# Performance work log

Measured on AMD Instinct MI355X. Metric: run time of the kernel, lower is better.

Reference implementation:

```python
import jax, jax.numpy as jnp
import numpy as np

LN_EPS = 1e-5

def _layernorm(x, gamma, beta):
    mu = jnp.mean(x, axis=-1, keepdims=True)
    var = jnp.var(x, axis=-1, keepdims=True)
    return (x - mu) * jax.lax.rsqrt(var + LN_EPS) * gamma + beta

def setup_inputs() -> dict:
    key = jax.random.key(0)
    ks = jax.random.split(key, 4)
    B, s, d, L = 8, 192, 512, 8
    h = 2048  # embed_dim * 2
    return {
        "lags": jax.random.normal(ks[0], (B, s, d, L), dtype=jnp.float32),
        "gamma1": jnp.ones((d,), jnp.float32),
        "beta1": jnp.zeros((d,), jnp.float32),
        "W1": jax.random.normal(ks[1], (d, h), jnp.float32) * (1.0 / np.sqrt(d)),
        "b1": jnp.zeros((h,), jnp.float32),
        "W2": jax.random.normal(ks[2], (h, d), jnp.float32) * (1.0 / np.sqrt(h)),
        "b2": jnp.zeros((d,), jnp.float32),
        "gamma3": jnp.ones((d,), jnp.float32),
        "beta3": jnp.zeros((d,), jnp.float32),
    }

def reference(lags, gamma1, beta1, W1, b1, W2, b2, gamma3, beta3):
    B, s, d, L = lags.shape
    # (B, s, d, L) -> (B, s, L, d) -> (B, S=s*L, d)
    x = jnp.transpose(lags, (0, 1, 3, 2)).reshape(B, s * L, d)
    scale = 1.0 / jnp.sqrt(jnp.asarray(d, x.dtype))
    # single-head, unprojected attention: scores = X X^T / sqrt(d)
    scores = jnp.einsum('bqd,bkd->bqk', x, x) * scale  # [B, S, S]
    attn = jax.nn.softmax(scores, axis=-1)
    attn_out = jnp.einsum('bqk,bkd->bqd', attn, x)
    q = _layernorm(x + attn_out, gamma1, beta1)
    ff = jnp.dot(jax.nn.gelu(jnp.dot(q, W1) + b1, approximate=False), W2) + b2
    out = _layernorm(q + ff, gamma3, beta3)
    # (B, S, d) -> (B, s, L, d) -> (B, s, d, L)
    return jnp.transpose(out.reshape(B, s, L, d), (0, 1, 3, 2))
```

## Files before the change

### kernel.cpp

```cpp
#include <hip/hip_runtime.h>
#include <hip/hip_bf16.h>
#include <math.h>

#define B_ 8
#define S_ 192
#define D_ 512
#define L_ 8
#define SQ 1536
#define H_ 2048
#define NROW (B_*SQ)
#define SCALE_QK 0.04419417382415922f

typedef unsigned short ushort_t;
typedef unsigned int uint_t;
typedef __attribute__((ext_vector_type(8))) short bf16x8;
typedef __attribute__((ext_vector_type(4))) float f32x4;

__device__ __forceinline__ float bfu2f(ushort_t u) { return __uint_as_float((unsigned)u << 16); }
__device__ __forceinline__ ushort_t f2bfu(float f) {
  __hip_bfloat16 h = __float2bfloat16(f);
  return *reinterpret_cast<ushort_t*>(&h);
}

__device__ __forceinline__ float gelu_fast(float x) {
  float z = fabsf(x) * 0.70710678118654752f;
  float t = __builtin_amdgcn_rcpf(fmaf(0.3275911f, z, 1.0f));
  float p = fmaf(1.061405429f, t, -1.453152027f);
  p = fmaf(p, t, 1.421413741f);
  p = fmaf(p, t, -0.284496736f);
  p = fmaf(p, t, 0.254829592f);
  p = p * t;
  float e = __expf(-z * z);
  float erfz = fmaf(-p, e, 1.0f);
  float s = (x >= 0.0f) ? erfz : -erfz;
  return 0.5f * x * (1.0f + s);
}

__device__ __forceinline__ void gl_lds16(const ushort_t* g, ushort_t* l) {
  __builtin_amdgcn_global_load_lds(
      (const __attribute__((address_space(1))) unsigned int*)g,
      (__attribute__((address_space(3))) unsigned int*)l, 16, 0, 0);
}

#define VMWAIT(N) asm volatile("s_waitcnt vmcnt(" #N ")" ::: "memory")

__global__ __launch_bounds__(256) void k_build_x_f(const float* __restrict__ lags,
                                                   float* __restrict__ x,
                                                   ushort_t* __restrict__ x_bf) {
  __shared__ float tile[512][9];
  const int tid = threadIdx.x;
  const float* in = lags + (size_t)blockIdx.x * 4096;
  #pragma unroll
  for (int it = 0; it < 4; ++it) {
    int f = (tid + it * 256) * 4;
    float4 v = *reinterpret_cast<const float4*>(in + f);
    int k = f >> 3, l0 = f & 7;
    tile[k][l0] = v.x; tile[k][l0 + 1] = v.y; tile[k][l0 + 2] = v.z; tile[k][l0 + 3] = v.w;
  }
  __syncthreads();
  const int l = tid >> 5, kbase = tid & 31;
  const size_t r = (size_t)blockIdx.x * 8 + l;
  #pragma unroll
  for (int j = 0; j < 16; ++j) {
    int k = kbase + 32 * j;
    float v = tile[k][l];
    x[r * D_ + k] = v;
    x_bf[r * D_ + k] = f2bfu(v);
  }
}

__global__ __launch_bounds__(256) void k_xt(const ushort_t* __restrict__ x_bf,
                                            ushort_t* __restrict__ xT) {
  __shared__ ushort_t tile[64][65];
  int t0 = blockIdx.x * 64, d0 = blockIdx.y * 64;
  const ushort_t* X = x_bf + (size_t)blockIdx.z * SQ * D_;
  ushort_t* XT = xT + (size_t)blockIdx.z * SQ * D_;
  for (int i = threadIdx.x; i < 4096; i += 256) {
    int tt = i >> 6, dd = i & 63;
    tile[dd][tt] = X[(size_t)(t0 + tt) * D_ + d0 + dd];
  }
  __syncthreads();
  for (int i = threadIdx.x; i < 4096; i += 256) {
    int dd = i >> 6, tt = i & 63;
    XT[(size_t)(d0 + dd) * SQ + t0 + tt] = tile[dd][tt];
  }
}

__global__ __launch_bounds__(256) void k_wt(const float* __restrict__ W,
                                            ushort_t* __restrict__ Wt,
                                            int K, int N) {
  __shared__ ushort_t tile[64][65];
  int n0 = blockIdx.x * 64, k0 = blockIdx.y * 64;
  for (int i = threadIdx.x; i < 4096; i += 256) {
    int kk = i >> 6, nn = i & 63;
    tile[nn][kk] = f2bfu(W[(size_t)(k0 + kk) * N + n0 + nn]);
  }
  __syncthreads();
  for (int i = threadIdx.x; i < 4096; i += 256) {
    int nn = i >> 6, kk = i & 63;
    Wt[(size_t)(n0 + nn) * K + k0 + kk] = tile[nn][kk];
  }
}

template<int MODE>
__global__ __launch_bounds__(256) void k_gemm(const ushort_t* __restrict__ A,
                                              const ushort_t* __restrict__ Bt,
                                              const float* __restrict__ bias,
                                              void* __restrict__ Cout,
                                              int M, int K, int N,
                                              size_t sAz, size_t sBz, size_t sCz,
                                              float scale) {
  A  += (size_t)blockIdx.z * sAz;
  Bt += (size_t)blockIdx.z * sBz;
  __shared__ ushort_t As0[128 * 64];
  __shared__ ushort_t As1[128 * 64];
  __shared__ ushort_t Bs0[128 * 64];
  __shared__ ushort_t Bs1[128 * 64];
  const int tid = threadIdx.x;
  const int m0 = blockIdx.y * 128, n0 = blockIdx.x * 128;
  const int w = tid >> 6, lane = tid & 63;
  const int wr = w >> 1, wc = w & 1;
  const int l15 = lane & 15, quad = lane >> 4;
  const int lrow8 = lane >> 3;
  const int cg = ((lane & 7) ^ lrow8) * 8;
  const int xsw = l15 & 7;
  const int lbase = (w * 32) * 64;
  const size_t sK8 = (size_t)8 * K;

  f32x4 acc[4][4];
  if (MODE <= 1) {
    #pragma unroll
    for (int nj = 0; nj < 4; ++nj) {
      float bv = bias[n0 + wc * 64 + nj * 16 + l15];
      #pragma unroll
      for (int mi = 0; mi < 4; ++mi) acc[mi][nj] = (f32x4){bv, bv, bv, bv};
    }
  } else {
    #pragma unroll
    for (int nj = 0; nj < 4; ++nj)
      #pragma unroll
      for (int mi = 0; mi < 4; ++mi) acc[mi][nj] = (f32x4){0.f, 0.f, 0.f, 0.f};
  }

  const ushort_t* gA = A  + (size_t)(m0 + w * 32 + lrow8) * K + cg;
  const ushort_t* gB = Bt + (size_t)(n0 + w * 32 + lrow8) * K + cg;

#define STAGE(AS, BS) do {                                                  \
    ushort_t* la_ = &AS[lbase]; ushort_t* lb_ = &BS[lbase];                 \
    _Pragma("unroll")                                                       \
    for (int j_ = 0; j_ < 4; ++j_) {                                        \
      gl_lds16(gA + (size_t)j_ * sK8, la_ + j_ * 8 * 64);                   \
      gl_lds16(gB + (size_t)j_ * sK8, lb_ + j_ * 8 * 64);                   \
    }                                                                       \
    gA += 64; gB += 64;                                                     \
  } while (0)

#define COMPUTE(AS, BS) do {                                                \
    _Pragma("unroll")                                                       \
    for (int kk_ = 0; kk_ < 2; ++kk_) {                                     \
      const int csel_ = ((kk_ * 4 + quad) ^ xsw) * 8;                       \
      bf16x8 af_[4], bf_[4];                                                \
      _Pragma("unroll")                                                     \
      for (int mi_ = 0; mi_ < 4; ++mi_)                                     \
        af_[mi_] = *reinterpret_cast<const bf16x8*>(                        \
            &AS[(wr * 64 + mi_ * 16 + l15) * 64 + csel_]);                  \
      _Pragma("unroll")                                                     \
      for (int nj_ = 0; nj_ < 4; ++nj_)                                     \
        bf_[nj_] = *reinterpret_cast<const bf16x8*>(                        \
            &BS[(wc * 64 + nj_ * 16 + l15) * 64 + csel_]);                  \
      _Pragma("unroll")                                                     \
      for (int mi_ = 0; mi_ < 4; ++mi_)                                     \
        _Pragma("unroll")                                                   \
        for (int nj_ = 0; nj_ < 4; ++nj_)                                   \
          acc[mi_][nj_] = __builtin_amdgcn_mfma_f32_16x16x32_bf16(          \
              af_[mi_], bf_[nj_], acc[mi_][nj_], 0, 0, 0);                  \
    }                                                                       \
  } while (0)

  STAGE(As0, Bs0);
  STAGE(As1, Bs1);

  const int nt = K >> 6;
  for (int t = 0; t < nt - 2; t += 2) {
    VMWAIT(8);
    __builtin_amdgcn_s_barrier();
    COMPUTE(As0, Bs0);
    __builtin_amdgcn_s_barrier();
    STAGE(As0, Bs0);
    VMWAIT(8);
    __builtin_amdgcn_s_barrier();
    COMPUTE(As1, Bs1);
    __builtin_amdgcn_s_barrier();
    STAGE(As1, Bs1);
  }
  VMWAIT(8);
  __builtin_amdgcn_s_barrier();
  COMPUTE(As0, Bs0);
  VMWAIT(0);
  __builtin_amdgcn_s_barrier();
  COMPUTE(As1, Bs1);

#undef STAGE
#undef COMPUTE

  ushort_t* Cb = (ushort_t*)Cout + (size_t)blockIdx.z * sCz;
  float*    Cf = (float*)Cout    + (size_t)blockIdx.z * sCz;
  #pragma unroll
  for (int mi = 0; mi < 4; ++mi)
    #pragma unroll
    for (int nj = 0; nj < 4; ++nj) {
      int gc = n0 + wc * 64 + nj * 16 + l15;
      #pragma unroll
      for (int r = 0; r < 4; ++r) {
        int gr = m0 + wr * 64 + mi * 16 + quad * 4 + r;
        float v = acc[mi][nj][r];
        if (MODE == 0) {
          Cb[(size_t)gr * N + gc] = f2bfu(gelu_fast(v));
        } else if (MODE == 1) {
          Cf[(size_t)gr * N + gc] = v;
        } else if (MODE == 2) {
          Cb[(size_t)gr * N + gc] = f2bfu(v * scale);
        } else {
          Cf[(size_t)gr * N + gc] = v;
        }
      }
    }
}

__global__ __launch_bounds__(256) void k_softmax_bf(ushort_t* __restrict__ sc) {
  uint_t* row = (uint_t*)(sc + (size_t)blockIdx.z * SQ * SQ + (size_t)blockIdx.x * SQ);
  int tid = threadIdx.x;
  __shared__ float red[8];
  float v[6];
  float m = -1e30f;
  #pragma unroll
  for (int k = 0; k < 3; ++k) {
    uint_t u = row[tid + k * 256];
    v[2*k]   = __uint_as_float(u << 16);
    v[2*k+1] = __uint_as_float(u & 0xffff0000u);
    m = fmaxf(m, fmaxf(v[2*k], v[2*k+1]));
  }
  #pragma unroll
  for (int o = 32; o > 0; o >>= 1) m = fmaxf(m, __shfl_down(m, o));
  if ((tid & 63) == 0) red[tid >> 6] = m;
  __syncthreads();
  m = fmaxf(fmaxf(red[0], red[1]), fmaxf(red[2], red[3]));
  __syncthreads();
  float ssum = 0.f;
  #pragma unroll
  for (int k = 0; k < 6; ++k) { v[k] = expf(v[k] - m); ssum += v[k]; }
  #pragma unroll
  for (int o = 32; o > 0; o >>= 1) ssum += __shfl_down(ssum, o);
  if ((tid & 63) == 0) red[4 + (tid >> 6)] = ssum;
  __syncthreads();
  float inv = 1.0f / (red[4] + red[5] + red[6] + red[7]);
  #pragma unroll
  for (int k = 0; k < 3; ++k) {
    uint_t lo = f2bfu(v[2*k] * inv);
    uint_t hi = f2bfu(v[2*k+1] * inv);
    row[tid + k * 256] = (hi << 16) | lo;
  }
}

__global__ __launch_bounds__(256) void k_ln1b(const float* __restrict__ x,
                                              const float* __restrict__ attn,
                                              const float* __restrict__ g,
                                              const float* __restrict__ be,
                                              ushort_t* __restrict__ qbf) {
  size_t base = (size_t)blockIdx.x * D_;
  int tid = threadIdx.x;
  __shared__ float rl[8];
  float v0 = x[base + tid] + attn[base + tid];
  float v1 = x[base + tid + 256] + attn[base + tid + 256];
  float s = v0 + v1, sq = v0 * v0 + v1 * v1;
  #pragma unroll
  for (int o = 32; o > 0; o >>= 1) { s += __shfl_down(s, o); sq += __shfl_down(sq, o); }
  int lane = tid & 63, wid = tid >> 6;
  if (lane == 0) { rl[wid] = s; rl[4 + wid] = sq; }
  __syncthreads();
  s = rl[0] + rl[1] + rl[2] + rl[3];
  sq = rl[4] + rl[5] + rl[6] + rl[7];
  float mean = s * (1.0f / 512.0f);
  float var = sq * (1.0f / 512.0f) - mean * mean;
  float rstd = rsqrtf(var + 1e-5f);
  qbf[base + tid]       = f2bfu((v0 - mean) * rstd * g[tid] + be[tid]);
  qbf[base + tid + 256] = f2bfu((v1 - mean) * rstd * g[tid + 256] + be[tid + 256]);
}

__global__ __launch_bounds__(256) void k_ln3_f(const float* __restrict__ y,
                                               const ushort_t* __restrict__ qbf,
                                               const float* __restrict__ g3,
                                               const float* __restrict__ be3,
                                               float* __restrict__ out) {
  __shared__ float ynorm[8][512];
  const int tid = threadIdx.x;
  const int w = tid >> 6, lane = tid & 63;
  #pragma unroll
  for (int rr = 0; rr < 2; ++rr) {
    int l = 2 * w + rr;
    size_t t = (size_t)blockIdx.x * 8 + l;
    float v[8];
    float s = 0.f, sq = 0.f;
    #pragma unroll
    for (int j = 0; j < 8; ++j) {
      int k = lane + 64 * j;
      v[j] = y[t * D_ + k] + bfu2f(qbf[t * D_ + k]);
      s += v[j]; sq += v[j] * v[j];
    }
    #pragma unroll
    for (int o = 32; o > 0; o >>= 1) { s += __shfl_down(s, o); sq += __shfl_down(sq, o); }
    s = __shfl(s, 0); sq = __shfl(sq, 0);
    float mean = s * (1.0f / 512.0f);
    float var = sq * (1.0f / 512.0f) - mean * mean;
    float rstd = rsqrtf(var + 1e-5f);
    #pragma unroll
    for (int j = 0; j < 8; ++j) {
      int k = lane + 64 * j;
      ynorm[l][k] = (v[j] - mean) * rstd * g3[k] + be3[k];
    }
  }
  __syncthreads();
  float* ob = out + (size_t)blockIdx.x * 4096;
  #pragma unroll
  for (int kk = 0; kk < 2; ++kk) {
    int k = tid * 2 + kk;
    float4 lo = make_float4(ynorm[0][k], ynorm[1][k], ynorm[2][k], ynorm[3][k]);
    float4 hi = make_float4(ynorm[4][k], ynorm[5][k], ynorm[6][k], ynorm[7][k]);
    *reinterpret_cast<float4*>(ob + (size_t)k * 8)     = lo;
    *reinterpret_cast<float4*>(ob + (size_t)k * 8 + 4) = hi;
  }
}

#define TS 64
#define KT 16
__global__ __launch_bounds__(256) void k_build_x_s(const float* __restrict__ lags,
                                                   float* __restrict__ x, int b_base) {
  int idx = blockIdx.x * 256 + threadIdx.x;
  int k = idx & (D_ - 1);
  int r = idx >> 9;
  int b = b_base + r / SQ;
  int t = r - (r / SQ) * SQ;
  int si = t >> 3, l = t & 7;
  size_t src = (((size_t)(b * S_ + si) * D_ + k) << 3) + l;
  x[idx] = lags[src];
}

__global__ __launch_bounds__(256) void k_scores(const float* __restrict__ x,
                                                float* __restrict__ sc, int b_base) {
  const float* A = x;
  float* C = sc;
  __shared__ float As[TS][KT + 1];
  __shared__ float Bs[TS][KT + 1];
  int tx = threadIdx.x & 15, ty = threadIdx.x >> 4;
  int j0 = blockIdx.x * TS, i0 = blockIdx.y * TS;
  float acc[4][4] = {};
  int lk = threadIdx.x & 15, lr = threadIdx.x >> 4;
  for (int k0 = 0; k0 < D_; k0 += KT) {
    #pragma unroll
    for (int it = 0; it < 4; ++it) {
      As[lr + 16 * it][lk] = A[(size_t)(i0 + lr + 16 * it) * D_ + k0 + lk];
      Bs[lr + 16 * it][lk] = A[(size_t)(j0 + lr + 16 * it) * D_ + k0 + lk];
    }
    __syncthreads();
    #pragma unroll
    for (int kk = 0; kk < KT; ++kk) {
      float a[4], bb[4];
      #pragma unroll
      for (int r = 0; r < 4; ++r) a[r] = As[ty * 4 + r][kk];
      #pragma unroll
      for (int c = 0; c < 4; ++c) bb[c] = Bs[tx * 4 + c][kk];
      #pragma unroll
      for (int r = 0; r < 4; ++r)
        #pragma unroll
        for (int c = 0; c < 4; ++c) acc[r][c] = fmaf(a[r], bb[c], acc[r][c]);
    }
    __syncthreads();
  }
  #pragma unroll
  for (int r = 0; r < 4; ++r) {
    float4 v = make_float4(acc[r][0]*SCALE_QK, acc[r][1]*SCALE_QK,
                           acc[r][2]*SCALE_QK, acc[r][3]*SCALE_QK);
    *reinterpret_cast<float4*>(&C[(size_t)(i0 + ty*4 + r) * SQ + j0 + tx*4]) = v;
  }
}

__global__ __launch_bounds__(256) void k_softmax(float* __restrict__ sc) {
  float* row = sc + (size_t)blockIdx.x * SQ;
  int tid = threadIdx.x;
  __shared__ float red[8];
  float m = -1e30f;
  for (int j = tid; j < SQ; j += 256) m = fmaxf(m, row[j]);
  #pragma unroll
  for (int o = 32; o > 0; o >>= 1) m = fmaxf(m, __shfl_down(m, o));
  if ((tid & 63) == 0) red[tid >> 6] = m;
  __syncthreads();
  m = fmaxf(fmaxf(red[0], red[1]), fmaxf(red[2], red[3]));
  __syncthreads();
  float ssum = 0.f;
  for (int j = tid; j < SQ; j += 256) { float e = expf(row[j] - m); row[j] = e; ssum += e; }
  #pragma unroll
  for (int o = 32; o > 0; o >>= 1) ssum += __shfl_down(ssum, o);
  if ((tid & 63) == 0) red[4 + (tid >> 6)] = ssum;
  __syncthreads();
  float inv = 1.0f / (red[4] + red[5] + red[6] + red[7]);
  for (int j = tid; j < SQ; j += 256) row[j] *= inv;
}

__global__ __launch_bounds__(256) void k_attn(const float* __restrict__ x,
                                              const float* __restrict__ sc,
                                              float* __restrict__ attn) {
  const float* X = x;
  const float* P = sc;
  float* O = attn;
  __shared__ float Ps[TS][KT + 1];
  __shared__ float Xs[KT][TS];
  int tx = threadIdx.x & 15, ty = threadIdx.x >> 4;
  int j0 = blockIdx.x * TS, i0 = blockIdx.y * TS;
  float acc[4][4] = {};
  int lk = threadIdx.x & 15, lr = threadIdx.x >> 4;
  int lc = threadIdx.x & 63, lrow = threadIdx.x >> 6;
  for (int k0 = 0; k0 < SQ; k0 += KT) {
    #pragma unroll
    for (int it = 0; it < 4; ++it)
      Ps[lr + 16 * it][lk] = P[(size_t)(i0 + lr + 16 * it) * SQ + k0 + lk];
    #pragma unroll
    for (int it = 0; it < 4; ++it)
      Xs[lrow + 4 * it][lc] = X[(size_t)(k0 + lrow + 4 * it) * D_ + j0 + lc];
    __syncthreads();
    #pragma unroll
    for (int kk = 0; kk < KT; ++kk) {
      float a[4], bb[4];
      #pragma unroll
      for (int r = 0; r < 4; ++r) a[r] = Ps[ty * 4 + r][kk];
      #pragma unroll
      for (int c = 0; c < 4; ++c) bb[c] = Xs[kk][tx * 4 + c];
      #pragma unroll
      for (int r = 0; r < 4; ++r)
        #pragma unroll
        for (int c = 0; c < 4; ++c) acc[r][c] = fmaf(a[r], bb[c], acc[r][c]);
    }
    __syncthreads();
  }
  #pragma unroll
  for (int r = 0; r < 4; ++r) {
    float4 v = make_float4(acc[r][0], acc[r][1], acc[r][2], acc[r][3]);
    *reinterpret_cast<float4*>(&O[(size_t)(i0 + ty*4 + r) * D_ + j0 + tx*4]) = v;
  }
}

__global__ __launch_bounds__(256) void k_ln1(const float* __restrict__ x,
                                             const float* __restrict__ attn,
                                             const float* __restrict__ g,
                                             const float* __restrict__ be,
                                             float* __restrict__ qout) {
  size_t base = (size_t)blockIdx.x * D_;
  int tid = threadIdx.x;
  __shared__ float rl[8];
  float v0 = x[base + tid] + attn[base + tid];
  float v1 = x[base + tid + 256] + attn[base + tid + 256];
  float s = v0 + v1, sq = v0 * v0 + v1 * v1;
  #pragma unroll
  for (int o = 32; o > 0; o >>= 1) { s += __shfl_down(s, o); sq += __shfl_down(sq, o); }
  int lane = tid & 63, wid = tid >> 6;
  if (lane == 0) { rl[wid] = s; rl[4 + wid] = sq; }
  __syncthreads();
  s = rl[0] + rl[1] + rl[2] + rl[3];
  sq = rl[4] + rl[5] + rl[6] + rl[7];
  float mean = s * (1.0f / 512.0f);
  float var = sq * (1.0f / 512.0f) - mean * mean;
  float rstd = rsqrtf(var + 1e-5f);
  qout[base + tid]       = (v0 - mean) * rstd * g[tid] + be[tid];
  qout[base + tid + 256] = (v1 - mean) * rstd * g[tid + 256] + be[tid + 256];
}

__global__ __launch_bounds__(256, 2) void k_ffn(
    const float* __restrict__ q,
    const float* __restrict__ W1, const float* __restrict__ b1,
    const float* __restrict__ W2, const float* __restrict__ b2,
    const float* __restrict__ g3, const float* __restrict__ be3,
    float* __restrict__ out, int row_base)
{
  __shared__ float qs[8][D_];
  __shared__ float mid[8][H_];
  const int tid = threadIdx.x;
  const int row0 = blockIdx.x * 8;
  for (int idx = tid; idx < 8 * D_; idx += 256)
    qs[idx >> 9][idx & (D_ - 1)] = q[(size_t)row0 * D_ + idx];
  __syncthreads();
  float acc[8][8];
  {
    float4 bA = *reinterpret_cast<const float4*>(b1 + (tid << 3));
    float4 bB = *reinterpret_cast<const float4*>(b1 + (tid << 3) + 4);
    float bv[8] = {bA.x, bA.y, bA.z, bA.w, bB.x, bB.y, bB.z, bB.w};
    #pragma unroll
    for (int jj = 0; jj < 8; ++jj)
      #pragma unroll
      for (int r = 0; r < 8; ++r) acc[jj][r] = bv[jj];
  }
  for (int k4 = 0; k4 < D_ / 4; ++k4) {
    float4 qv[8];
    #pragma unroll
    for (int r = 0; r < 8; ++r)
      qv[r] = *reinterpret_cast<const float4*>(&qs[r][k4 << 2]);
    #pragma unroll
    for (int kk = 0; kk < 4; ++kk) {
      const int k = (k4 << 2) + kk;
      float4 wA = *reinterpret_cast<const float4*>(W1 + (size_t)k * H_ + (tid << 3));
      float4 wB = *reinterpret_cast<const float4*>(W1 + (size_t)k * H_ + (tid << 3) + 4);
      float wv[8] = {wA.x, wA.y, wA.z, wA.w, wB.x, wB.y, wB.z, wB.w};
      #pragma unroll
      for (int r = 0; r < 8; ++r) {
        float qk = (kk == 0) ? qv[r].x : (kk == 1) ? qv[r].y : (kk == 2) ? qv[r].z : qv[r].w;
        #pragma unroll
        for (int jj = 0; jj < 8; ++jj) acc[jj][r] = fmaf(qk, wv[jj], acc[jj][r]);
      }
    }
  }
  #pragma unroll
  for (int jj = 0; jj < 8; ++jj)
    #pragma unroll
    for (int r = 0; r < 8; ++r) {
      float v = acc[jj][r];
      mid[r][(tid << 3) + jj] = 0.5f * v * (1.0f + erff(v * 0.70710678118654752f));
    }
  __syncthreads();
  float acc2[8][2];
  {
    float b20 = b2[tid << 1], b21 = b2[(tid << 1) + 1];
    #pragma unroll
    for (int r = 0; r < 8; ++r) { acc2[r][0] = b20; acc2[r][1] = b21; }
  }
  for (int j4 = 0; j4 < H_ / 4; ++j4) {
    float4 mv[8];
    #pragma unroll
    for (int r = 0; r < 8; ++r)
      mv[r] = *reinterpret_cast<const float4*>(&mid[r][j4 << 2]);
    #pragma unroll
    for (int kk = 0; kk < 4; ++kk) {
      const int j = (j4 << 2) + kk;
      float2 wv = *reinterpret_cast<const float2*>(W2 + (size_t)j * D_ + (tid << 1));
      #pragma unroll
      for (int r = 0; r < 8; ++r) {
        float m = (kk == 0) ? mv[r].x : (kk == 1) ? mv[r].y : (kk == 2) ? mv[r].z : mv[r].w;
        acc2[r][0] = fmaf(m, wv.x, acc2[r][0]);
        acc2[r][1] = fmaf(m, wv.y, acc2[r][1]);
      }
    }
  }
  __syncthreads();
  float* ys = &mid[0][0];
  #pragma unroll
  for (int r = 0; r < 8; ++r) {
    ys[r * D_ + (tid << 1)]     = qs[r][(tid << 1)]     + acc2[r][0];
    ys[r * D_ + (tid << 1) + 1] = qs[r][(tid << 1) + 1] + acc2[r][1];
  }
  __syncthreads();
  float g3a = g3[tid],  g3b = g3[tid + 256];
  float be3a = be3[tid], be3b = be3[tid + 256];
  float* rl = &qs[0][0];
  for (int r = 0; r < 8; ++r) {
    float v0 = ys[r * D_ + tid], v1 = ys[r * D_ + tid + 256];
    float s = v0 + v1, sq = v0 * v0 + v1 * v1;
    #pragma unroll
    for (int o = 32; o > 0; o >>= 1) { s += __shfl_down(s, o); sq += __shfl_down(sq, o); }
    int lane = tid & 63, wid = tid >> 6;
    if (lane == 0) { rl[wid] = s; rl[4 + wid] = sq; }
    __syncthreads();
    s = rl[0] + rl[1] + rl[2] + rl[3];
    sq = rl[4] + rl[5] + rl[6] + rl[7];
    __syncthreads();
    float mean = s * (1.0f / 512.0f);
    float var = sq * (1.0f / 512.0f) - mean * mean;
    float rstd = rsqrtf(var + 1e-5f);
    int t = row_base + row0 + r;
    int b = t / SQ, tt = t - b * SQ;
    int si = tt >> 3, l = tt & 7;
    size_t ob = (((size_t)(b * S_ + si) * D_) << 3) + l;
    out[ob + ((size_t)tid << 3)]         = (v0 - mean) * rstd * g3a + be3a;
    out[ob + ((size_t)(tid + 256) << 3)] = (v1 - mean) * rstd * g3b + be3b;
  }
}

extern "C" void kernel_launch(void* const* d_in, const int* in_sizes, int n_in,
                              void* d_out, int out_size, void* d_ws, size_t ws_size,
                              hipStream_t stream) {
  const float* lags   = (const float*)d_in[0];
  const float* gamma1 = (const float*)d_in[1];
  const float* beta1  = (const float*)d_in[2];
  const float* W1     = (const float*)d_in[3];
  const float* b1     = (const float*)d_in[4];
  const float* W2     = (const float*)d_in[5];
  const float* b2     = (const float*)d_in[6];
  const float* g3     = (const float*)d_in[7];
  const float* be3    = (const float*)d_in[8];
  float* out = (float*)d_out;

  float* ws = (float*)d_ws;
  const size_t NX  = (size_t)B_ * SQ * D_;
  const size_t NXB = (size_t)SQ * D_;
  const size_t NS  = (size_t)SQ * SQ;

  const size_t need_full = (3 * NX + 8 * NS) * sizeof(float);

  if (ws_size >= need_full) {
    float* x        = ws;
    float* attn     = x + NX;
    ushort_t* q_bf  = (ushort_t*)(attn + NX);
    ushort_t* w1t   = q_bf + NX;
    ushort_t* w2t   = w1t + (size_t)H_ * D_;
    ushort_t* region = w2t + (size_t)H_ * D_;
    ushort_t* sc_bf = region;
    ushort_t* x_bf  = region + 8 * NS;
    ushort_t* xT_bf = x_bf + NX;
    ushort_t* mid_bf = region;

    k_build_x_f<<<dim3(B_ * S_), 256, 0, stream>>>(lags, x, x_bf);
    k_xt<<<dim3(SQ / 64, D_ / 64, B_), 256, 0, stream>>>(x_bf, xT_bf);
    k_wt<<<dim3(H_ / 64, D_ / 64), 256, 0, stream>>>(W1, w1t, D_, H_);
    k_wt<<<dim3(D_ / 64, H_ / 64), 256, 0, stream>>>(W2, w2t, H_, D_);
    k_gemm<2><<<dim3(SQ / 128, SQ / 128, B_), 256, 0, stream>>>(
        x_bf, x_bf, nullptr, sc_bf, SQ, D_, SQ, NXB, NXB, NS, SCALE_QK);
    k_softmax_bf<<<dim3(SQ, 1, B_), 256, 0, stream>>>(sc_bf);
    k_gemm<3><<<dim3(D_ / 128, SQ / 128, B_), 256, 0, stream>>>(
        sc_bf, xT_bf, nullptr, attn, SQ, SQ, D_, NS, NXB, NXB, 1.0f);
    k_ln1b<<<dim3(NROW), 256, 0, stream>>>(x, attn, gamma1, beta1, q_bf);
    k_gemm<0><<<dim3(H_ / 128, NROW / 128, 1), 256, 0, stream>>>(
        q_bf, w1t, b1, mid_bf, NROW, D_, H_, 0, 0, 0, 1.0f);
    k_gemm<1><<<dim3(D_ / 128, NROW / 128, 1), 256, 0, stream>>>(
        mid_bf, w2t, b2, attn, NROW, H_, D_, 0, 0, 0, 1.0f);
    k_ln3_f<<<dim3(B_ * S_), 256, 0, stream>>>(attn, q_bf, g3, be3, out);
  } else {
    float* xb   = ws;
    float* sc   = xb + NXB;
    float* atb  = sc + NS;
    float* qb   = atb + NXB;
    for (int b = 0; b < B_; ++b) {
      k_build_x_s<<<dim3((unsigned)(NXB / 256)), 256, 0, stream>>>(lags, xb, b);
      k_scores<<<dim3(SQ / TS, SQ / TS, 1), 256, 0, stream>>>(xb, sc, b);
      k_softmax<<<dim3(SQ, 1, 1), 256, 0, stream>>>(sc);
      k_attn<<<dim3(D_ / TS, SQ / TS, 1), 256, 0, stream>>>(xb, sc, atb);
      k_ln1<<<dim3(SQ), 256, 0, stream>>>(xb, atb, gamma1, beta1, qb);
      k_ffn<<<dim3(SQ / 8), 256, 0, stream>>>(qb, W1, b1, W2, b2, g3, be3, out, b * SQ);
    }
  }
}
```

Measured before the change: 299.2 us.

## Switch GEMMs to 32x32 MFMA, fuse X transpose into build, use tanh GELU

The GEMM kernel now uses 32x32x16 bf16 MFMA with 2x2 accumulator tiles per wave instead of 4x4 tiles of 16x16x32, and the LDS read swizzle and epilogue index mapping are adjusted to match. The separate transpose kernel for X is removed, and the build kernel writes the transposed bf16 copy directly from its shared tile, saving a launch and a global round trip. The erf-based GELU is replaced by the tanh approximation to cut instruction count, which slightly changes the numerics relative to exact GELU.

```diff
diff --git a/kernel.cpp b/kernel.cpp
--- a/kernel.cpp
+++ b/kernel.cpp
@@ -15,6 +15,7 @@
 typedef unsigned int uint_t;
 typedef __attribute__((ext_vector_type(8))) short bf16x8;
 typedef __attribute__((ext_vector_type(4))) float f32x4;
+typedef __attribute__((ext_vector_type(16))) float f32x16;
 
 __device__ __forceinline__ float bfu2f(ushort_t u) { return __uint_as_float((unsigned)u << 16); }
 __device__ __forceinline__ ushort_t f2bfu(float f) {
@@ -22,18 +23,13 @@
   return *reinterpret_cast<ushort_t*>(&h);
 }
 
-__device__ __forceinline__ float gelu_fast(float x) {
-  float z = fabsf(x) * 0.70710678118654752f;
-  float t = __builtin_amdgcn_rcpf(fmaf(0.3275911f, z, 1.0f));
-  float p = fmaf(1.061405429f, t, -1.453152027f);
-  p = fmaf(p, t, 1.421413741f);
-  p = fmaf(p, t, -0.284496736f);
-  p = fmaf(p, t, 0.254829592f);
-  p = p * t;
-  float e = __expf(-z * z);
-  float erfz = fmaf(-p, e, 1.0f);
-  float s = (x >= 0.0f) ? erfz : -erfz;
-  return 0.5f * x * (1.0f + s);
+__device__ __forceinline__ float gelu_tanh(float x) {
+  float x2 = x * x;
+  float u2 = x * fmaf(0.0713548162f, x2, 1.5957691216f);
+  float e = __expf(u2);
+  float r = fmaf(-2.0f, __builtin_amdgcn_rcpf(e + 1.0f), 1.0f);
+  float hx = 0.5f * x;
+  return fmaf(hx, r, hx);
 }
 
 __device__ __forceinline__ void gl_lds16(const ushort_t* g, ushort_t* l) {
@@ -46,7 +42,8 @@
 
 __global__ __launch_bounds__(256) void k_build_x_f(const float* __restrict__ lags,
                                                    float* __restrict__ x,
-                                                   ushort_t* __restrict__ x_bf) {
+                                                   ushort_t* __restrict__ x_bf,
+                                                   ushort_t* __restrict__ xT) {
   __shared__ float tile[512][9];
   const int tid = threadIdx.x;
   const float* in = lags + (size_t)blockIdx.x * 4096;
@@ -67,22 +64,19 @@
     x[r * D_ + k] = v;
     x_bf[r * D_ + k] = f2bfu(v);
   }
-}
-
-__global__ __launch_bounds__(256) void k_xt(const ushort_t* __restrict__ x_bf,
-                                            ushort_t* __restrict__ xT) {
-  __shared__ ushort_t tile[64][65];
-  int t0 = blockIdx.x * 64, d0 = blockIdx.y * 64;
-  const ushort_t* X = x_bf + (size_t)blockIdx.z * SQ * D_;
-  ushort_t* XT = xT + (size_t)blockIdx.z * SQ * D_;
-  for (int i = threadIdx.x; i < 4096; i += 256) {
-    int tt = i >> 6, dd = i & 63;
-    tile[dd][tt] = X[(size_t)(t0 + tt) * D_ + d0 + dd];
-  }
-  __syncthreads();
-  for (int i = threadIdx.x; i < 4096; i += 256) {
-    int dd = i >> 6, tt = i & 63;
-    XT[(size_t)(d0 + dd) * SQ + t0 + tt] = tile[dd][tt];
+  const int b = blockIdx.x / S_, si = blockIdx.x - b * S_;
+  #pragma unroll
+  for (int dd = 0; dd < 2; ++dd) {
+    int d = tid + dd * 256;
+    uint_t pk[4];
+    #pragma unroll
+    for (int j = 0; j < 4; ++j) {
+      uint_t lo = f2bfu(tile[d][2 * j]);
+      uint_t hi = f2bfu(tile[d][2 * j + 1]);
+      pk[j] = (hi << 16) | lo;
+    }
+    uint_t* dst = (uint_t*)(xT + ((size_t)b * D_ + d) * SQ + si * 8);
+    *reinterpret_cast<uint4*>(dst) = make_uint4(pk[0], pk[1], pk[2], pk[3]);
   }
 }
 
@@ -120,26 +114,29 @@
   const int m0 = blockIdx.y * 128, n0 = blockIdx.x * 128;
   const int w = tid >> 6, lane = tid & 63;
   const int wr = w >> 1, wc = w & 1;
-  const int l15 = lane & 15, quad = lane >> 4;
+  const int l31 = lane & 31, khi = lane >> 5, x7 = lane & 7;
   const int lrow8 = lane >> 3;
   const int cg = ((lane & 7) ^ lrow8) * 8;
-  const int xsw = l15 & 7;
   const int lbase = (w * 32) * 64;
   const size_t sK8 = (size_t)8 * K;
 
-  f32x4 acc[4][4];
+  f32x16 acc[2][2];
   if (MODE <= 1) {
     #pragma unroll
-    for (int nj = 0; nj < 4; ++nj) {
-      float bv = bias[n0 + wc * 64 + nj * 16 + l15];
-      #pragma unroll
-      for (int mi = 0; mi < 4; ++mi) acc[mi][nj] = (f32x4){bv, bv, bv, bv};
+    for (int nj = 0; nj < 2; ++nj) {
+      float bv = bias[n0 + wc * 64 + nj * 32 + l31];
+      #pragma unroll
+      for (int mi = 0; mi < 2; ++mi)
+        #pragma unroll
+        for (int rg = 0; rg < 16; ++rg) acc[mi][nj][rg] = bv;
     }
   } else {
     #pragma unroll
-    for (int nj = 0; nj < 4; ++nj)
-      #pragma unroll
-      for (int mi = 0; mi < 4; ++mi) acc[mi][nj] = (f32x4){0.f, 0.f, 0.f, 0.f};
+    for (int nj = 0; nj < 2; ++nj)
+      #pragma unroll
+      for (int mi = 0; mi < 2; ++mi)
+        #pragma unroll
+        for (int rg = 0; rg < 16; ++rg) acc[mi][nj][rg] = 0.f;
   }
 
   const ushort_t* gA = A  + (size_t)(m0 + w * 32 + lrow8) * K + cg;
@@ -157,22 +154,22 @@
 
 #define COMPUTE(AS, BS) do {                                                \
     _Pragma("unroll")                                                       \
-    for (int kk_ = 0; kk_ < 2; ++kk_) {                                     \
-      const int csel_ = ((kk_ * 4 + quad) ^ xsw) * 8;                       \
-      bf16x8 af_[4], bf_[4];                                                \
+    for (int ks_ = 0; ks_ < 4; ++ks_) {                                     \
+      const int pos_ = ((ks_ * 2 + khi) ^ x7) * 8;                          \
+      bf16x8 af_[2], bf_[2];                                                \
       _Pragma("unroll")                                                     \
-      for (int mi_ = 0; mi_ < 4; ++mi_)                                     \
+      for (int mi_ = 0; mi_ < 2; ++mi_)                                     \
         af_[mi_] = *reinterpret_cast<const bf16x8*>(                        \
-            &AS[(wr * 64 + mi_ * 16 + l15) * 64 + csel_]);                  \
+            &AS[(wr * 64 + mi_ * 32 + l31) * 64 + pos_]);                   \
       _Pragma("unroll")                                                     \
-      for (int nj_ = 0; nj_ < 4; ++nj_)                                     \
+      for (int nj_ = 0; nj_ < 2; ++nj_)                                     \
         bf_[nj_] = *reinterpret_cast<const bf16x8*>(                        \
-            &BS[(wc * 64 + nj_ * 16 + l15) * 64 + csel_]);                  \
+            &BS[(wc * 64 + nj_ * 32 + l31) * 64 + pos_]);                   \
       _Pragma("unroll")                                                     \
-      for (int mi_ = 0; mi_ < 4; ++mi_)                                     \
+      for (int mi_ = 0; mi_ < 2; ++mi_)                                     \
         _Pragma("unroll")                                                   \
-        for (int nj_ = 0; nj_ < 4; ++nj_)                                   \
-          acc[mi_][nj_] = __builtin_amdgcn_mfma_f32_16x16x32_bf16(          \
+        for (int nj_ = 0; nj_ < 2; ++nj_)                                   \
+          acc[mi_][nj_] = __builtin_amdgcn_mfma_f32_32x32x16_bf16(          \
               af_[mi_], bf_[nj_], acc[mi_][nj_], 0, 0, 0);                  \
     }                                                                       \
   } while (0)
@@ -206,16 +203,16 @@
   ushort_t* Cb = (ushort_t*)Cout + (size_t)blockIdx.z * sCz;
   float*    Cf = (float*)Cout    + (size_t)blockIdx.z * sCz;
   #pragma unroll
-  for (int mi = 0; mi < 4; ++mi)
-    #pragma unroll
-    for (int nj = 0; nj < 4; ++nj) {
-      int gc = n0 + wc * 64 + nj * 16 + l15;
-      #pragma unroll
-      for (int r = 0; r < 4; ++r) {
-        int gr = m0 + wr * 64 + mi * 16 + quad * 4 + r;
-        float v = acc[mi][nj][r];
+  for (int mi = 0; mi < 2; ++mi)
+    #pragma unroll
+    for (int nj = 0; nj < 2; ++nj) {
+      int gc = n0 + wc * 64 + nj * 32 + l31;
+      #pragma unroll
+      for (int rg = 0; rg < 16; ++rg) {
+        int gr = m0 + wr * 64 + mi * 32 + (rg & 3) + 8 * (rg >> 2) + 4 * khi;
+        float v = acc[mi][nj][rg];
         if (MODE == 0) {
-          Cb[(size_t)gr * N + gc] = f2bfu(gelu_fast(v));
+          Cb[(size_t)gr * N + gc] = f2bfu(gelu_tanh(v));
         } else if (MODE == 1) {
           Cf[(size_t)gr * N + gc] = v;
         } else if (MODE == 2) {
@@ -614,8 +611,7 @@
     ushort_t* xT_bf = x_bf + NX;
     ushort_t* mid_bf = region;
 
-    k_build_x_f<<<dim3(B_ * S_), 256, 0, stream>>>(lags, x, x_bf);
-    k_xt<<<dim3(SQ / 64, D_ / 64, B_), 256, 0, stream>>>(x_bf, xT_bf);
+    k_build_x_f<<<dim3(B_ * S_), 256, 0, stream>>>(lags, x, x_bf, xT_bf);
     k_wt<<<dim3(H_ / 64, D_ / 64), 256, 0, stream>>>(W1, w1t, D_, H_);
     k_wt<<<dim3(D_ / 64, H_ / 64), 256, 0, stream>>>(W2, w2t, H_, D_);
     k_gemm<2><<<dim3(SQ / 128, SQ / 128, B_), 256, 0, stream>>>(
```

Result: no change. 298.0 us (-0.4%).

## Fuse softmax into QK GEMM epilogue, defer normalization, fold X transpose into build

Applied to the files above, without the earlier changes.

The standalone softmax kernel is removed. The QK^T GEMM epilogue now computes exp2 of the scaled scores with no max subtraction, stores them as bf16 and atomically accumulates per-row sums. The PV GEMM then divides by those sums in its epilogue. The transposed bf16 X is written directly by the build kernel, dropping the separate transpose kernel. GELU switches from an erf polynomial to a tanh approximation. This saves one full read-write pass over the score matrix and two launches, at the cost of atomics, a zeroing kernel, and an overflow risk from skipping the max subtraction, which is only safe for bounded inputs.

```diff
diff --git a/kernel.cpp b/kernel.cpp
--- a/kernel.cpp
+++ b/kernel.cpp
@@ -10,6 +10,7 @@
 #define H_ 2048
 #define NROW (B_*SQ)
 #define SCALE_QK 0.04419417382415922f
+#define SCALE_QK2 0.06377551974755906f
 
 typedef unsigned short ushort_t;
 typedef unsigned int uint_t;
@@ -22,18 +23,13 @@
   return *reinterpret_cast<ushort_t*>(&h);
 }
 
-__device__ __forceinline__ float gelu_fast(float x) {
-  float z = fabsf(x) * 0.70710678118654752f;
-  float t = __builtin_amdgcn_rcpf(fmaf(0.3275911f, z, 1.0f));
-  float p = fmaf(1.061405429f, t, -1.453152027f);
-  p = fmaf(p, t, 1.421413741f);
-  p = fmaf(p, t, -0.284496736f);
-  p = fmaf(p, t, 0.254829592f);
-  p = p * t;
-  float e = __expf(-z * z);
-  float erfz = fmaf(-p, e, 1.0f);
-  float s = (x >= 0.0f) ? erfz : -erfz;
-  return 0.5f * x * (1.0f + s);
+__device__ __forceinline__ float gelu_tanh(float x) {
+  float x2 = x * x;
+  float u2 = x * fmaf(0.0713548162f, x2, 1.5957691216f);
+  float e = __expf(u2);
+  float r = fmaf(-2.0f, __builtin_amdgcn_rcpf(e + 1.0f), 1.0f);
+  float hx = 0.5f * x;
+  return fmaf(hx, r, hx);
 }
 
 __device__ __forceinline__ void gl_lds16(const ushort_t* g, ushort_t* l) {
@@ -44,9 +40,14 @@
 
 #define VMWAIT(N) asm volatile("s_waitcnt vmcnt(" #N ")" ::: "memory")
 
+__global__ __launch_bounds__(256) void k_zero(float* __restrict__ p) {
+  p[(size_t)blockIdx.x * 256 + threadIdx.x] = 0.f;
+}
+
 __global__ __launch_bounds__(256) void k_build_x_f(const float* __restrict__ lags,
                                                    float* __restrict__ x,
-                                                   ushort_t* __restrict__ x_bf) {
+                                                   ushort_t* __restrict__ x_bf,
+                                                   ushort_t* __restrict__ xT) {
   __shared__ float tile[512][9];
   const int tid = threadIdx.x;
   const float* in = lags + (size_t)blockIdx.x * 4096;
@@ -67,22 +68,19 @@
     x[r * D_ + k] = v;
     x_bf[r * D_ + k] = f2bfu(v);
   }
-}
-
-__global__ __launch_bounds__(256) void k_xt(const ushort_t* __restrict__ x_bf,
-                                            ushort_t* __restrict__ xT) {
-  __shared__ ushort_t tile[64][65];
-  int t0 = blockIdx.x * 64, d0 = blockIdx.y * 64;
-  const ushort_t* X = x_bf + (size_t)blockIdx.z * SQ * D_;
-  ushort_t* XT = xT + (size_t)blockIdx.z * SQ * D_;
-  for (int i = threadIdx.x; i < 4096; i += 256) {
-    int tt = i >> 6, dd = i & 63;
-    tile[dd][tt] = X[(size_t)(t0 + tt) * D_ + d0 + dd];
-  }
-  __syncthreads();
-  for (int i = threadIdx.x; i < 4096; i += 256) {
-    int dd = i >> 6, tt = i & 63;
-    XT[(size_t)(d0 + dd) * SQ + t0 + tt] = tile[dd][tt];
+  const int b = blockIdx.x / S_, si = blockIdx.x - b * S_;
+  #pragma unroll
+  for (int dd = 0; dd < 2; ++dd) {
+    int d = tid + dd * 256;
+    uint_t pk[4];
+    #pragma unroll
+    for (int j = 0; j < 4; ++j) {
+      uint_t lo = f2bfu(tile[d][2 * j]);
+      uint_t hi = f2bfu(tile[d][2 * j + 1]);
+      pk[j] = (hi << 16) | lo;
+    }
+    uint_t* dst = (uint_t*)(xT + ((size_t)b * D_ + d) * SQ + si * 8);
+    *reinterpret_cast<uint4*>(dst) = make_uint4(pk[0], pk[1], pk[2], pk[3]);
   }
 }
 
@@ -106,6 +104,7 @@
 __global__ __launch_bounds__(256) void k_gemm(const ushort_t* __restrict__ A,
                                               const ushort_t* __restrict__ Bt,
                                               const float* __restrict__ bias,
+                                              float* __restrict__ rsums,
                                               void* __restrict__ Cout,
                                               int M, int K, int N,
                                               size_t sAz, size_t sBz, size_t sCz,
@@ -205,60 +204,49 @@
 
   ushort_t* Cb = (ushort_t*)Cout + (size_t)blockIdx.z * sCz;
   float*    Cf = (float*)Cout    + (size_t)blockIdx.z * sCz;
-  #pragma unroll
-  for (int mi = 0; mi < 4; ++mi)
-    #pragma unroll
-    for (int nj = 0; nj < 4; ++nj) {
-      int gc = n0 + wc * 64 + nj * 16 + l15;
+
+  if (MODE == 4) {
+    float* rs = rsums + (size_t)blockIdx.z * SQ;
+    #pragma unroll
+    for (int mi = 0; mi < 4; ++mi)
       #pragma unroll
       for (int r = 0; r < 4; ++r) {
         int gr = m0 + wr * 64 + mi * 16 + quad * 4 + r;
-        float v = acc[mi][nj][r];
-        if (MODE == 0) {
-          Cb[(size_t)gr * N + gc] = f2bfu(gelu_fast(v));
-        } else if (MODE == 1) {
-          Cf[(size_t)gr * N + gc] = v;
-        } else if (MODE == 2) {
-          Cb[(size_t)gr * N + gc] = f2bfu(v * scale);
-        } else {
-          Cf[(size_t)gr * N + gc] = v;
+        float s = 0.f;
+        #pragma unroll
+        for (int nj = 0; nj < 4; ++nj) {
+          int gc = n0 + wc * 64 + nj * 16 + l15;
+          float e = exp2f(acc[mi][nj][r] * scale);
+          ushort_t ub = f2bfu(e);
+          Cb[(size_t)gr * N + gc] = ub;
+          s += bfu2f(ub);
+        }
+        #pragma unroll
+        for (int m_ = 1; m_ < 16; m_ <<= 1) s += __shfl_xor(s, m_);
+        if (l15 == 0) atomicAdd(&rs[gr], s);
+      }
+  } else {
+    const float* rs = rsums + (size_t)blockIdx.z * SQ;
+    #pragma unroll
+    for (int mi = 0; mi < 4; ++mi)
+      #pragma unroll
+      for (int nj = 0; nj < 4; ++nj) {
+        int gc = n0 + wc * 64 + nj * 16 + l15;
+        #pragma unroll
+        for (int r = 0; r < 4; ++r) {
+          int gr = m0 + wr * 64 + mi * 16 + quad * 4 + r;
+          float v = acc[mi][nj][r];
+          if (MODE == 0) {
+            Cb[(size_t)gr * N + gc] = f2bfu(gelu_tanh(v));
+          } else if (MODE == 1) {
+            Cf[(size_t)gr * N + gc] = v;
+          } else if (MODE == 5) {
+            Cf[(size_t)gr * N + gc] = v * __builtin_amdgcn_rcpf(rs[gr]);
+          } else {
+            Cf[(size_t)gr * N + gc] = v;
+          }
         }
       }
-    }
-}
-
-__global__ __launch_bounds__(256) void k_softmax_bf(ushort_t* __restrict__ sc) {
-  uint_t* row = (uint_t*)(sc + (size_t)blockIdx.z * SQ * SQ + (size_t)blockIdx.x * SQ);
-  int tid = threadIdx.x;
-  __shared__ float red[8];
-  float v[6];
-  float m = -1e30f;
-  #pragma unroll
-  for (int k = 0; k < 3; ++k) {
-    uint_t u = row[tid + k * 256];
-    v[2*k]   = __uint_as_float(u << 16);
-    v[2*k+1] = __uint_as_float(u & 0xffff0000u);
-    m = fmaxf(m, fmaxf(v[2*k], v[2*k+1]));
-  }
-  #pragma unroll
-  for (int o = 32; o > 0; o >>= 1) m = fmaxf(m, __shfl_down(m, o));
-  if ((tid & 63) == 0) red[tid >> 6] = m;
-  __syncthreads();
-  m = fmaxf(fmaxf(red[0], red[1]), fmaxf(red[2], red[3]));
-  __syncthreads();
-  float ssum = 0.f;
-  #pragma unroll
-  for (int k = 0; k < 6; ++k) { v[k] = expf(v[k] - m); ssum += v[k]; }
-  #pragma unroll
-  for (int o = 32; o > 0; o >>= 1) ssum += __shfl_down(ssum, o);
-  if ((tid & 63) == 0) red[4 + (tid >> 6)] = ssum;
-  __syncthreads();
-  float inv = 1.0f / (red[4] + red[5] + red[6] + red[7]);
-  #pragma unroll
-  for (int k = 0; k < 3; ++k) {
-    uint_t lo = f2bfu(v[2*k] * inv);
-    uint_t hi = f2bfu(v[2*k+1] * inv);
-    row[tid + k * 256] = (hi << 16) | lo;
   }
 }
 
@@ -608,26 +596,26 @@
     ushort_t* q_bf  = (ushort_t*)(attn + NX);
     ushort_t* w1t   = q_bf + NX;
     ushort_t* w2t   = w1t + (size_t)H_ * D_;
-    ushort_t* region = w2t + (size_t)H_ * D_;
+    float* rowsum   = (float*)(w2t + (size_t)H_ * D_);
+    ushort_t* region = (ushort_t*)(rowsum + (size_t)B_ * SQ);
     ushort_t* sc_bf = region;
     ushort_t* x_bf  = region + 8 * NS;
     ushort_t* xT_bf = x_bf + NX;
     ushort_t* mid_bf = region;
 
-    k_build_x_f<<<dim3(B_ * S_), 256, 0, stream>>>(lags, x, x_bf);
-    k_xt<<<dim3(SQ / 64, D_ / 64, B_), 256, 0, stream>>>(x_bf, xT_bf);
+    k_build_x_f<<<dim3(B_ * S_), 256, 0, stream>>>(lags, x, x_bf, xT_bf);
     k_wt<<<dim3(H_ / 64, D_ / 64), 256, 0, stream>>>(W1, w1t, D_, H_);
     k_wt<<<dim3(D_ / 64, H_ / 64), 256, 0, stream>>>(W2, w2t, H_, D_);
-    k_gemm<2><<<dim3(SQ / 128, SQ / 128, B_), 256, 0, stream>>>(
-        x_bf, x_bf, nullptr, sc_bf, SQ, D_, SQ, NXB, NXB, NS, SCALE_QK);
-    k_softmax_bf<<<dim3(SQ, 1, B_), 256, 0, stream>>>(sc_bf);
-    k_gemm<3><<<dim3(D_ / 128, SQ / 128, B_), 256, 0, stream>>>(
-        sc_bf, xT_bf, nullptr, attn, SQ, SQ, D_, NS, NXB, NXB, 1.0f);
+    k_zero<<<dim3(B_ * SQ / 256), 256, 0, stream>>>(rowsum);
+    k_gemm<4><<<dim3(SQ / 128, SQ / 128, B_), 256, 0, stream>>>(
+        x_bf, x_bf, nullptr, rowsum, sc_bf, SQ, D_, SQ, NXB, NXB, NS, SCALE_QK2);
+    k_gemm<5><<<dim3(D_ / 128, SQ / 128, B_), 256, 0, stream>>>(
+        sc_bf, xT_bf, nullptr, rowsum, attn, SQ, SQ, D_, NS, NXB, NXB, 1.0f);
     k_ln1b<<<dim3(NROW), 256, 0, stream>>>(x, attn, gamma1, beta1, q_bf);
     k_gemm<0><<<dim3(H_ / 128, NROW / 128, 1), 256, 0, stream>>>(
-        q_bf, w1t, b1, mid_bf, NROW, D_, H_, 0, 0, 0, 1.0f);
+        q_bf, w1t, b1, nullptr, mid_bf, NROW, D_, H_, 0, 0, 0, 1.0f);
     k_gemm<1><<<dim3(D_ / 128, NROW / 128, 1), 256, 0, stream>>>(
-        mid_bf, w2t, b2, attn, NROW, H_, D_, 0, 0, 0, 1.0f);
+        mid_bf, w2t, b2, nullptr, attn, NROW, H_, D_, 0, 0, 0, 1.0f);
     k_ln3_f<<<dim3(B_ * S_), 256, 0, stream>>>(attn, q_bf, g3, be3, out);
   } else {
     float* xb   = ws;
```

Measured after the change: 294.6 us. No clear change (-1.5%).
